# Performance work log

Hardware: AMD Instinct MI355X
Metric: run time of the kernel (lower is better)

Reference implementation:

```python
import jax, jax.numpy as jnp
import numpy as np

SIGMA = 1.0  # init kwarg: Gaussian kernel width

B, P, F = 8192, 8192, 256


def setup_inputs() -> dict:
    key = jax.random.key(0)
    kx, kp = jax.random.split(key)
    x = jax.random.normal(kx, (B, F), dtype=jnp.float32)
    prototypes = jax.random.normal(kp, (P, F), dtype=jnp.float32)
    return {"x": x, "prototypes": prototypes}


def reference(x, prototypes):
    x_sq = jnp.sum(x * x, axis=-1, keepdims=True)            # [B,1]
    p_sq = jnp.sum(prototypes * prototypes, axis=-1)          # [P]
    cross = jnp.einsum('bf,pf->bp', x, prototypes)            # [B,P]
    d2 = jnp.maximum(x_sq + p_sq[None, :] - 2.0 * cross, 0.0)
    # NOTE: original takes .pow(0.5) -> euclidean NORM (despite variable name)
    dist = jnp.sqrt(d2)                                       # [B,P]
    denom = jnp.float32(2.0 * SIGMA ** 2)
    return jnp.exp(-dist / denom)
```

## Files before the change

### kernel.cpp

```cpp
#include <hip/hip_runtime.h>
#include <cstdint>
#include <cstddef>

#define B_ROWS 8192
#define P_ROWS 8192
#define FDIM   256

#define BAND    128
#define STRIP   1024
#define TILE    64
#define NTILES  (STRIP / TILE)
#define NBANDS  (B_ROWS / BAND)
#define NSTRIPS (P_ROWS / STRIP)

typedef __bf16  bf16x8  __attribute__((ext_vector_type(8)));
typedef float   floatx4 __attribute__((ext_vector_type(4)));

__device__ __forceinline__ unsigned short f2bf(float f) {
  unsigned int u = __float_as_uint(f);
  u += 0x7fffu + ((u >> 16) & 1u);
  return (unsigned short)(u >> 16);
}

__device__ __forceinline__ void async16(const void* g, void* l) {
  __builtin_amdgcn_global_load_lds(
      (const __attribute__((address_space(1))) void*)g,
      (__attribute__((address_space(3))) void*)l,
      16, 0, 0);
}

__global__ void __launch_bounds__(64) prep_kernel(
    const float* __restrict__ x, const float* __restrict__ p,
    unsigned short* __restrict__ xbf, unsigned short* __restrict__ pbf,
    float* __restrict__ x2, float* __restrict__ p2) {
  const int row  = blockIdx.x;
  const int lane = threadIdx.x;

  const float* src;
  unsigned short* dst;
  float* nrm;
  int r;
  if (row < B_ROWS) { src = x; dst = xbf; nrm = x2; r = row; }
  else              { src = p; dst = pbf; nrm = p2; r = row - B_ROWS; }

  const float4 v = *reinterpret_cast<const float4*>(src + (size_t)r * FDIM + lane * 4);
  float s = v.x * v.x + v.y * v.y + v.z * v.z + v.w * v.w;
  #pragma unroll
  for (int o = 32; o > 0; o >>= 1) s += __shfl_down(s, o);
  if (lane == 0) nrm[r] = s;

  ushort4 pk;
  pk.x = f2bf(v.x); pk.y = f2bf(v.y); pk.z = f2bf(v.z); pk.w = f2bf(v.w);
  *reinterpret_cast<ushort4*>(dst + (size_t)r * FDIM + lane * 4) = pk;
}

__global__ void __launch_bounds__(256, 2) gauss_kernel(
    const unsigned short* __restrict__ xbf, const unsigned short* __restrict__ pbf,
    const float* __restrict__ x2, const float* __restrict__ p2,
    float* __restrict__ out) {
  __shared__ __align__(16) unsigned short lds_b[2][TILE * FDIM];

  const int t    = threadIdx.x;
  const int lane = t & 63;
  const int w    = t >> 6;
  const int lm   = lane & 15;
  const int q    = lane >> 4;
  const int s3   = lm & 7;

  const int band  = blockIdx.x & (NBANDS - 1);
  const int strip = blockIdx.x >> 6;
  const int M0  = band * BAND;
  const int N0s = strip * STRIP;

  const int rowA = M0 + w * 32 + lm;
  bf16x8 af[2][8];
  #pragma unroll
  for (int i = 0; i < 2; ++i)
    #pragma unroll
    for (int kw = 0; kw < 8; ++kw)
      af[i][kw] = *(const bf16x8*)&xbf[(size_t)(rowA + i * 16) * FDIM + kw * 32 + q * 8];

  floatx4 x2v[2];
  #pragma unroll
  for (int i = 0; i < 2; ++i)
    x2v[i] = *(const floatx4*)&x2[M0 + w * 32 + i * 16 + q * 4];

  unsigned int bOff[8];
  unsigned int ldsOff[8];
  #pragma unroll
  for (int I = 0; I < 8; ++I) {
    const int L = I * 256 + w * 64 + lane;
    const int r = L >> 5;
    const int c = L & 31;
    const int g = (c & 24) | ((c ^ r) & 7);
    const int pl = 4 * (r & 15) + (r >> 4);
    bOff[I]   = (unsigned int)((((N0s + pl) * FDIM) + g * 8) * 2);
    ldsOff[I] = (unsigned int)((I * 256 + w * 64) * 16);
  }
  const char* pbfB = (const char*)pbf;

  unsigned int oOff[2][4];
  #pragma unroll
  for (int i = 0; i < 2; ++i)
    #pragma unroll
    for (int v = 0; v < 4; ++v)
      oOff[i][v] = (unsigned int)(((M0 + w * 32 + i * 16 + q * 4 + v) * (size_t)P_ROWS
                                   + (N0s + 4 * lm)) * 4);

  #pragma unroll
  for (int I = 0; I < 8; ++I)
    async16(pbfB + bOff[I], (char*)&lds_b[0][0] + ldsOff[I]);
  asm volatile("s_waitcnt vmcnt(0)" ::: "memory");
  __builtin_amdgcn_s_barrier();

  for (int tt = 0; tt < NTILES; ++tt) {
    const int cur = tt & 1;
    const floatx4 p2r = *(const floatx4*)&p2[N0s + tt * TILE + 4 * lm];

    if (tt < NTILES - 1) {
      #pragma unroll
      for (int I = 0; I < 8; ++I)
        async16(pbfB + bOff[I] + (unsigned int)((tt + 1) * (TILE * FDIM * 2)),
                (char*)&lds_b[cur ^ 1][0] + ldsOff[I]);
    }

    floatx4 acc[2][4] = {};
    const unsigned short* lb = &lds_b[cur][0];
    #pragma unroll
    for (int kw = 0; kw < 8; ++kw) {
      bf16x8 bfr[4];
      #pragma unroll
      for (int j = 0; j < 4; ++j) {
        const int cc = (kw * 4 + q) ^ s3;
        bfr[j] = *(const bf16x8*)&lb[(j * 16 + lm) * FDIM + cc * 8];
      }
      #pragma unroll
      for (int i = 0; i < 2; ++i)
        #pragma unroll
        for (int j = 0; j < 4; ++j)
          acc[i][j] = __builtin_amdgcn_mfma_f32_16x16x32_bf16(af[i][kw], bfr[j], acc[i][j], 0, 0, 0);
    }

    #pragma unroll
    for (int i = 0; i < 2; ++i) {
      #pragma unroll
      for (int v = 0; v < 4; ++v) {
        floatx4 res;
        #pragma unroll
        for (int j = 0; j < 4; ++j) {
          float d2 = x2v[i][v] + p2r[j] - 2.0f * acc[i][j][v];
          d2 = fmaxf(d2, 0.0f);
          res[j] = __expf(-0.5f * sqrtf(d2));
        }
        __builtin_nontemporal_store(
            res, (floatx4*)((char*)out + oOff[i][v] + (unsigned int)(tt * (TILE * 4))));
      }
    }

    if (tt < NTILES - 1) {
      asm volatile("s_waitcnt vmcnt(8)" ::: "memory");
      __builtin_amdgcn_s_barrier();
    }
  }
}

extern "C" void kernel_launch(void* const* d_in, const int* in_sizes, int n_in,
                              void* d_out, int out_size, void* d_ws, size_t ws_size,
                              hipStream_t stream) {
  const float* x = (const float*)d_in[0];
  const float* p = (const float*)d_in[1];
  float* out = (float*)d_out;

  char* ws = (char*)d_ws;
  unsigned short* xbf = (unsigned short*)ws;
  unsigned short* pbf = (unsigned short*)(ws + (size_t)B_ROWS * FDIM * 2);
  float* x2 = (float*)(ws + (size_t)(B_ROWS + P_ROWS) * FDIM * 2);
  float* p2 = x2 + B_ROWS;

  prep_kernel<<<dim3(B_ROWS + P_ROWS), dim3(64), 0, stream>>>(x, p, xbf, pbf, x2, p2);

  gauss_kernel<<<dim3(NBANDS * NSTRIPS), dim3(256), 0, stream>>>(xbf, pbf, x2, p2, out);
}
```

Before: 341.7 us.

## Drop LDS staging, load prototype fragments directly from global with XCD-aware tiling

Removes the LDS double buffer and async global-to-LDS loads. Each wave now reads its prototype MFMA fragments straight from global memory, relying on L2 for reuse. Blocks are smaller (128x256 instead of 128x1024), so the grid is larger, and block indices are remapped so that each XCD owns a contiguous range of prototype columns for better L2 locality. The occupancy hint rises from 2 to 3 blocks per CU. The intent is to cut barrier and LDS overhead and improve occupancy, at the cost of redundant global/L2 reads across the four waves and possibly uncoalesced B-fragment loads.

Measured after the change: 388.9 us. 13.8% more time.

```diff
diff --git a/kernel.cpp b/kernel.cpp
--- a/kernel.cpp
+++ b/kernel.cpp
@@ -6,12 +6,10 @@
 #define P_ROWS 8192
 #define FDIM   256
 
-#define BAND    128
-#define STRIP   1024
-#define TILE    64
-#define NTILES  (STRIP / TILE)
-#define NBANDS  (B_ROWS / BAND)
-#define NSTRIPS (P_ROWS / STRIP)
+#define MB     128
+#define NB     256
+#define NTILES 4
+#define NBLK   ((B_ROWS / MB) * (P_ROWS / NB))
 
 typedef __bf16  bf16x8  __attribute__((ext_vector_type(8)));
 typedef float   floatx4 __attribute__((ext_vector_type(4)));
@@ -20,13 +18,6 @@
   unsigned int u = __float_as_uint(f);
   u += 0x7fffu + ((u >> 16) & 1u);
   return (unsigned short)(u >> 16);
-}
-
-__device__ __forceinline__ void async16(const void* g, void* l) {
-  __builtin_amdgcn_global_load_lds(
-      (const __attribute__((address_space(1))) void*)g,
-      (__attribute__((address_space(3))) void*)l,
-      16, 0, 0);
 }
 
 __global__ void __launch_bounds__(64) prep_kernel(
@@ -54,86 +45,50 @@
   *reinterpret_cast<ushort4*>(dst + (size_t)r * FDIM + lane * 4) = pk;
 }
 
-__global__ void __launch_bounds__(256, 2) gauss_kernel(
+__global__ void __launch_bounds__(256, 3) gauss_kernel(
     const unsigned short* __restrict__ xbf, const unsigned short* __restrict__ pbf,
     const float* __restrict__ x2, const float* __restrict__ p2,
     float* __restrict__ out) {
-  __shared__ __align__(16) unsigned short lds_b[2][TILE * FDIM];
-
   const int t    = threadIdx.x;
   const int lane = t & 63;
   const int w    = t >> 6;
   const int lm   = lane & 15;
   const int q    = lane >> 4;
-  const int s3   = lm & 7;
 
-  const int band  = blockIdx.x & (NBANDS - 1);
-  const int strip = blockIdx.x >> 6;
-  const int M0  = band * BAND;
-  const int N0s = strip * STRIP;
+  const int f   = blockIdx.x;
+  const int xcd = f & 7;
+  const int idx = f >> 3;
+  const int bm  = idx & 63;
+  const int bn  = xcd * 4 + (idx >> 6);
 
-  const int rowA = M0 + w * 32 + lm;
+  const int M0 = bm * MB + w * 32;
+  const int N0 = bn * NB;
+
+  const unsigned short* aBase = xbf + (size_t)(M0 + lm) * FDIM + q * 8;
   bf16x8 af[2][8];
   #pragma unroll
   for (int i = 0; i < 2; ++i)
     #pragma unroll
     for (int kw = 0; kw < 8; ++kw)
-      af[i][kw] = *(const bf16x8*)&xbf[(size_t)(rowA + i * 16) * FDIM + kw * 32 + q * 8];
+      af[i][kw] = *(const bf16x8*)(aBase + (size_t)i * 16 * FDIM + kw * 32);
 
   floatx4 x2v[2];
   #pragma unroll
   for (int i = 0; i < 2; ++i)
-    x2v[i] = *(const floatx4*)&x2[M0 + w * 32 + i * 16 + q * 4];
+    x2v[i] = *(const floatx4*)&x2[M0 + i * 16 + q * 4];
 
-  unsigned int bOff[8];
-  unsigned int ldsOff[8];
-  #pragma unroll
-  for (int I = 0; I < 8; ++I) {
-    const int L = I * 256 + w * 64 + lane;
-    const int r = L >> 5;
-    const int c = L & 31;
-    const int g = (c & 24) | ((c ^ r) & 7);
-    const int pl = 4 * (r & 15) + (r >> 4);
-    bOff[I]   = (unsigned int)((((N0s + pl) * FDIM) + g * 8) * 2);
-    ldsOff[I] = (unsigned int)((I * 256 + w * 64) * 16);
-  }
-  const char* pbfB = (const char*)pbf;
-
-  unsigned int oOff[2][4];
-  #pragma unroll
-  for (int i = 0; i < 2; ++i)
-    #pragma unroll
-    for (int v = 0; v < 4; ++v)
-      oOff[i][v] = (unsigned int)(((M0 + w * 32 + i * 16 + q * 4 + v) * (size_t)P_ROWS
-                                   + (N0s + 4 * lm)) * 4);
-
-  #pragma unroll
-  for (int I = 0; I < 8; ++I)
-    async16(pbfB + bOff[I], (char*)&lds_b[0][0] + ldsOff[I]);
-  asm volatile("s_waitcnt vmcnt(0)" ::: "memory");
-  __builtin_amdgcn_s_barrier();
+  const unsigned short* bBase = pbf + (size_t)(4 * lm) * FDIM + q * 8;
 
   for (int tt = 0; tt < NTILES; ++tt) {
-    const int cur = tt & 1;
-    const floatx4 p2r = *(const floatx4*)&p2[N0s + tt * TILE + 4 * lm];
-
-    if (tt < NTILES - 1) {
-      #pragma unroll
-      for (int I = 0; I < 8; ++I)
-        async16(pbfB + bOff[I] + (unsigned int)((tt + 1) * (TILE * FDIM * 2)),
-                (char*)&lds_b[cur ^ 1][0] + ldsOff[I]);
-    }
+    const int Nt = N0 + tt * 64;
 
     floatx4 acc[2][4] = {};
-    const unsigned short* lb = &lds_b[cur][0];
     #pragma unroll
     for (int kw = 0; kw < 8; ++kw) {
       bf16x8 bfr[4];
       #pragma unroll
-      for (int j = 0; j < 4; ++j) {
-        const int cc = (kw * 4 + q) ^ s3;
-        bfr[j] = *(const bf16x8*)&lb[(j * 16 + lm) * FDIM + cc * 8];
-      }
+      for (int j = 0; j < 4; ++j)
+        bfr[j] = *(const bf16x8*)(bBase + (size_t)(Nt + j) * FDIM + kw * 32);
       #pragma unroll
       for (int i = 0; i < 2; ++i)
         #pragma unroll
@@ -141,6 +96,7 @@
           acc[i][j] = __builtin_amdgcn_mfma_f32_16x16x32_bf16(af[i][kw], bfr[j], acc[i][j], 0, 0, 0);
     }
 
+    const floatx4 p2r = *(const floatx4*)&p2[Nt + 4 * lm];
     #pragma unroll
     for (int i = 0; i < 2; ++i) {
       #pragma unroll
@@ -153,13 +109,8 @@
           res[j] = __expf(-0.5f * sqrtf(d2));
         }
         __builtin_nontemporal_store(
-            res, (floatx4*)((char*)out + oOff[i][v] + (unsigned int)(tt * (TILE * 4))));
+            res, (floatx4*)(out + (size_t)(M0 + i * 16 + q * 4 + v) * P_ROWS + Nt + 4 * lm));
       }
-    }
-
-    if (tt < NTILES - 1) {
-      asm volatile("s_waitcnt vmcnt(8)" ::: "memory");
-      __builtin_amdgcn_s_barrier();
     }
   }
 }
@@ -179,5 +130,5 @@
 
   prep_kernel<<<dim3(B_ROWS + P_ROWS), dim3(64), 0, stream>>>(x, p, xbf, pbf, x2, p2);
 
-  gauss_kernel<<<dim3(NBANDS * NSTRIPS), dim3(256), 0, stream>>>(xbf, pbf, x2, p2, out);
+  gauss_kernel<<<dim3(NBLK), dim3(256), 0, stream>>>(xbf, pbf, x2, p2, out);
 }
```
